# Kernel tuning notes

Hardware: AMD Instinct MI355X
Metric: run time of the kernel (lower is better)

## Reference

```python
import jax, jax.numpy as jnp
import numpy as np

N, E = 100_000, 1_600_000
NFEAT, NHID, HEADS = 128, 128, 2
FOUT = NHID // 2  # per-head out feats (DGL GATConv(nfeat, nhid//2, num_heads=2))
NEG_SLOPE = 0.2
LN_EPS = 1e-5


def setup_inputs() -> dict:
    key = jax.random.key(0)
    ks = jax.random.split(key, 10)
    h = jax.random.normal(ks[0], (N, NFEAT), dtype=jnp.float32)
    src = jax.random.randint(ks[1], (E,), 0, N, dtype=jnp.int32)
    dst = jax.random.randint(ks[2], (E,), 0, N, dtype=jnp.int32)
    # GATConv params
    W = jax.random.normal(ks[3], (NFEAT, HEADS * FOUT), dtype=jnp.float32) / np.sqrt(NFEAT)
    attn_l = jax.random.normal(ks[4], (HEADS, FOUT), dtype=jnp.float32) * 0.1
    attn_r = jax.random.normal(ks[5], (HEADS, FOUT), dtype=jnp.float32) * 0.1
    bias = jnp.zeros((HEADS * FOUT,), dtype=jnp.float32)
    # LayerNorm params
    gamma = jnp.ones((NHID,), dtype=jnp.float32)
    beta = jnp.zeros((NHID,), dtype=jnp.float32)
    return {"h": h, "src": src, "dst": dst, "W": W, "attn_l": attn_l,
            "attn_r": attn_r, "bias": bias, "gamma": gamma, "beta": beta}


def reference(h, src, dst, W, attn_l, attn_r, bias, gamma, beta):
    # --- GATConv ---
    feat = (h @ W).reshape(N, HEADS, FOUT)                 # [N,H,F]
    el = jnp.einsum('nhf,hf->nh', feat, attn_l)            # [N,H]
    er = jnp.einsum('nhf,hf->nh', feat, attn_r)            # [N,H]
    e = jax.nn.leaky_relu(el[src] + er[dst], NEG_SLOPE)    # [E,H]
    # edge softmax over incoming edges of each dst node
    emax = jax.ops.segment_max(e, dst, num_segments=N)     # [N,H] (-inf for empty ok)
    expe = jnp.exp(e - emax[dst])                          # [E,H]
    denom = jax.ops.segment_sum(expe, dst, num_segments=N) # [N,H]
    alpha = expe / denom[dst]                              # [E,H]
    msg = feat[src] * alpha[:, :, None]                    # [E,H,F]
    out = jax.ops.segment_sum(msg, dst, num_segments=N)    # [N,H,F]
    x = out.reshape(N, HEADS * FOUT) + bias                # [N,NHID]
    # --- LayerNorm ---
    mu = jnp.mean(x, axis=-1, keepdims=True)
    var = jnp.mean(jnp.square(x - mu), axis=-1, keepdims=True)
    return gamma * (x - mu) * jax.lax.rsqrt(var + LN_EPS) + beta
```

## Files before the change

kernel.cpp:

```cpp
#include <hip/hip_runtime.h>
#include <hip/hip_bf16.h>

#define NFEAT 128
#define NHID  128
#define HEADS 2
#define FOUT  64
#define NEG_SLOPE 0.2f
#define LN_EPS 1e-5f
#define MAXE 256
#define NPART 4
#define PACK_BLOCKS 64
#define STRIDE 64

typedef __attribute__((ext_vector_type(8))) short  short8;
typedef __attribute__((ext_vector_type(4))) float  floatx4;
typedef unsigned short ushort_t;

__device__ __forceinline__ unsigned short f32_to_bf16_bits(float x) {
    unsigned int u = __float_as_uint(x);
    unsigned int r = (u + 0x7FFF + ((u >> 16) & 1)) >> 16;
    return (unsigned short)r;
}

__global__ __launch_bounds__(256) void histscatter_pack_kernel(
    const float* __restrict__ W, ushort_t* __restrict__ pBhi,
    ushort_t* __restrict__ pBlo, const int* __restrict__ src,
    const int* __restrict__ dst, int* __restrict__ deg,
    int* __restrict__ csr_src, int E, int N)
{
    if (blockIdx.x < PACK_BLOCKS) {
        int i = blockIdx.x * 256 + threadIdx.x;
        int k = i >> 7, n = i & 127;
        float x = W[i];
        unsigned short hb = f32_to_bf16_bits(x);
        float hf = __uint_as_float(((unsigned int)hb) << 16);
        unsigned short lb = f32_to_bf16_bits(x - hf);
        int t = n >> 4, s = k >> 5, q = (k >> 3) & 3, j = k & 7;
        int lanei = (q << 4) | (n & 15);
        int idx = ((t * 4 + s) * 64 + lanei) * 8 + j;
        pBhi[idx] = hb; pBlo[idx] = lb;
        return;
    }
    int bid   = blockIdx.x - PACK_BLOCKS;
    int p     = bid & (NPART - 1);
    int chunk = bid >> 2;
    int i = chunk * 256 + threadIdx.x;
    if (i >= E) return;
    int d = dst[i];
    int lo = (int)(((long long)p       * N) / NPART);
    int hi = (int)(((long long)(p + 1) * N) / NPART);
    if (d >= lo && d < hi) {
        int pos = atomicAdd(&deg[d], 1);
        if (pos < STRIDE)
            csr_src[(size_t)d * STRIDE + pos] = src[i];
    }
}

__global__ __launch_bounds__(256) void gemm_mfma_kernel(
    const float* __restrict__ h,
    const ushort_t* __restrict__ pBhi, const ushort_t* __restrict__ pBlo,
    const float* __restrict__ attn_l, const float* __restrict__ attn_r,
    ushort_t* __restrict__ featb, float* __restrict__ el,
    float* __restrict__ er, int N)
{
    const int lane = threadIdx.x & 63;
    const int wv   = threadIdx.x >> 6;
    const int r0   = blockIdx.x * 64 + wv * 16;
    const int m    = lane & 15;
    const int q    = lane >> 4;
    int row  = r0 + m;
    int rowc = min(row, N - 1);
    const float* hrow = h + (size_t)rowc * NFEAT + q * 8;

    floatx4 acc[8];
#pragma unroll
    for (int t = 0; t < 8; t++) acc[t] = (floatx4){0.f, 0.f, 0.f, 0.f};

#pragma unroll
    for (int s = 0; s < 4; ++s) {
        float4 a0 = *(const float4*)(hrow + s * 32);
        float4 a1 = *(const float4*)(hrow + s * 32 + 4);
        float af[8] = {a0.x, a0.y, a0.z, a0.w, a1.x, a1.y, a1.z, a1.w};
        short8 ahi, alo;
#pragma unroll
        for (int jj = 0; jj < 8; jj++) {
            unsigned short hb = f32_to_bf16_bits(af[jj]);
            float hf = __uint_as_float(((unsigned int)hb) << 16);
            unsigned short lb = f32_to_bf16_bits(af[jj] - hf);
            ahi[jj] = (short)hb; alo[jj] = (short)lb;
        }
#pragma unroll
        for (int t = 0; t < 8; t++) {
            short8 bhi = *(const short8*)(pBhi + ((t * 4 + s) * 64 + lane) * 8);
            short8 blo = *(const short8*)(pBlo + ((t * 4 + s) * 64 + lane) * 8);
            acc[t] = __builtin_amdgcn_mfma_f32_16x16x32_bf16(ahi, bhi, acc[t], 0, 0, 0);
            acc[t] = __builtin_amdgcn_mfma_f32_16x16x32_bf16(ahi, blo, acc[t], 0, 0, 0);
            acc[t] = __builtin_amdgcn_mfma_f32_16x16x32_bf16(alo, bhi, acc[t], 0, 0, 0);
        }
    }
    if (r0 >= N) return;

    float alc[8], arc[8];
#pragma unroll
    for (int t = 0; t < 8; t++) {
        alc[t] = attn_l[t * 16 + m];
        arc[t] = attn_r[t * 16 + m];
    }

#pragma unroll
    for (int r = 0; r < 4; r++) {
        int rr = r0 + q * 4 + r;
        bool ok = (rr < N);
        if (ok) {
#pragma unroll
            for (int t = 0; t < 8; t++)
                featb[(size_t)rr * NHID + t * 16 + m] = f32_to_bf16_bits(acc[t][r]);
        }
        float pl0 = 0.f, pl1 = 0.f, pr0 = 0.f, pr1 = 0.f;
#pragma unroll
        for (int t = 0; t < 4; t++) {
            pl0 += acc[t][r] * alc[t];
            pr0 += acc[t][r] * arc[t];
            pl1 += acc[t + 4][r] * alc[t + 4];
            pr1 += acc[t + 4][r] * arc[t + 4];
        }
#pragma unroll
        for (int off = 1; off < 16; off <<= 1) {
            pl0 += __shfl_xor(pl0, off, 64);
            pl1 += __shfl_xor(pl1, off, 64);
            pr0 += __shfl_xor(pr0, off, 64);
            pr1 += __shfl_xor(pr1, off, 64);
        }
        if (m == 0 && ok) {
            el[rr * HEADS + 0] = pl0;
            el[rr * HEADS + 1] = pl1;
            er[rr * HEADS + 0] = pr0;
            er[rr * HEADS + 1] = pr1;
        }
    }
}

__global__ __launch_bounds__(256) void aggregate_kernel(
    const int* __restrict__ deg_arr, const int* __restrict__ csr_src,
    const ushort_t* __restrict__ featb, const float* __restrict__ el,
    const float* __restrict__ er, const float* __restrict__ bias,
    const float* __restrict__ gamma, const float* __restrict__ beta,
    float* __restrict__ out, int N)
{
    __shared__ int    s_src[4][STRIDE];
    __shared__ float2 s_e[4][STRIDE];

    const int wv   = threadIdx.x >> 6;
    const int lane = threadIdx.x & 63;
    const int node = blockIdx.x * 4 + wv;
    if (node >= N) return;

    const int deg = min(deg_arr[node], STRIDE);
    const int rs  = node * STRIDE;
    const float2 erv = *(const float2*)(er + (size_t)node * HEADS);

    float d0 = 0.f, d1 = 0.f;
    if (lane < deg) {
        int s = csr_src[rs + lane];
        float2 elv = *(const float2*)(el + (size_t)s * HEADS);
        float e0 = elv.x + erv.x; e0 = e0 > 0.f ? e0 : NEG_SLOPE * e0;
        float e1 = elv.y + erv.y; e1 = e1 > 0.f ? e1 : NEG_SLOPE * e1;
        float x0 = __expf(e0), x1 = __expf(e1);
        s_src[wv][lane] = s;
        s_e[wv][lane] = make_float2(x0, x1);
        d0 = x0; d1 = x1;
    }
#pragma unroll
    for (int off = 32; off; off >>= 1) {
        d0 += __shfl_xor(d0, off, 64);
        d1 += __shfl_xor(d1, off, 64);
    }

    const int j0   = lane * 2;
    const int hsel = lane >> 5;
    const float* s_ef = (const float*)&s_e[wv][0];
    float acc0 = 0.f, acc1 = 0.f;
    {
        int i = 0;
        for (; i + 8 <= deg; i += 8) {
            int s0 = s_src[wv][i + 0], s1 = s_src[wv][i + 1];
            int s2 = s_src[wv][i + 2], s3 = s_src[wv][i + 3];
            int s4 = s_src[wv][i + 4], s5 = s_src[wv][i + 5];
            int s6 = s_src[wv][i + 6], s7 = s_src[wv][i + 7];
            unsigned int u0 = *(const unsigned int*)(featb + (size_t)s0 * NHID + j0);
            unsigned int u1 = *(const unsigned int*)(featb + (size_t)s1 * NHID + j0);
            unsigned int u2 = *(const unsigned int*)(featb + (size_t)s2 * NHID + j0);
            unsigned int u3 = *(const unsigned int*)(featb + (size_t)s3 * NHID + j0);
            unsigned int u4 = *(const unsigned int*)(featb + (size_t)s4 * NHID + j0);
            unsigned int u5 = *(const unsigned int*)(featb + (size_t)s5 * NHID + j0);
            unsigned int u6 = *(const unsigned int*)(featb + (size_t)s6 * NHID + j0);
            unsigned int u7 = *(const unsigned int*)(featb + (size_t)s7 * NHID + j0);
            float a0 = s_ef[2 * (i + 0) + hsel];
            float a1 = s_ef[2 * (i + 1) + hsel];
            float a2 = s_ef[2 * (i + 2) + hsel];
            float a3 = s_ef[2 * (i + 3) + hsel];
            float a4 = s_ef[2 * (i + 4) + hsel];
            float a5 = s_ef[2 * (i + 5) + hsel];
            float a6 = s_ef[2 * (i + 6) + hsel];
            float a7 = s_ef[2 * (i + 7) + hsel];
            acc0 += __uint_as_float(u0 << 16) * a0;
            acc1 += __uint_as_float(u0 & 0xFFFF0000u) * a0;
            acc0 += __uint_as_float(u1 << 16) * a1;
            acc1 += __uint_as_float(u1 & 0xFFFF0000u) * a1;
            acc0 += __uint_as_float(u2 << 16) * a2;
            acc1 += __uint_as_float(u2 & 0xFFFF0000u) * a2;
            acc0 += __uint_as_float(u3 << 16) * a3;
            acc1 += __uint_as_float(u3 & 0xFFFF0000u) * a3;
            acc0 += __uint_as_float(u4 << 16) * a4;
            acc1 += __uint_as_float(u4 & 0xFFFF0000u) * a4;
            acc0 += __uint_as_float(u5 << 16) * a5;
            acc1 += __uint_as_float(u5 & 0xFFFF0000u) * a5;
            acc0 += __uint_as_float(u6 << 16) * a6;
            acc1 += __uint_as_float(u6 & 0xFFFF0000u) * a6;
            acc0 += __uint_as_float(u7 << 16) * a7;
            acc1 += __uint_as_float(u7 & 0xFFFF0000u) * a7;
        }
        for (; i + 2 <= deg; i += 2) {
            int s0 = s_src[wv][i + 0], s1 = s_src[wv][i + 1];
            unsigned int u0 = *(const unsigned int*)(featb + (size_t)s0 * NHID + j0);
            unsigned int u1 = *(const unsigned int*)(featb + (size_t)s1 * NHID + j0);
            float a0 = s_ef[2 * (i + 0) + hsel];
            float a1 = s_ef[2 * (i + 1) + hsel];
            acc0 += __uint_as_float(u0 << 16) * a0;
            acc1 += __uint_as_float(u0 & 0xFFFF0000u) * a0;
            acc0 += __uint_as_float(u1 << 16) * a1;
            acc1 += __uint_as_float(u1 & 0xFFFF0000u) * a1;
        }
        for (; i < deg; ++i) {
            int s = s_src[wv][i];
            float a = s_ef[2 * i + hsel];
            unsigned int u = *(const unsigned int*)(featb + (size_t)s * NHID + j0);
            acc0 += __uint_as_float(u << 16) * a;
            acc1 += __uint_as_float(u & 0xFFFF0000u) * a;
        }
    }
    float inv = (deg > 0) ? 1.f / ((lane < 32) ? d0 : d1) : 0.f;

    float2 bv = *(const float2*)(bias + j0);
    float x0 = acc0 * inv + bv.x;
    float x1 = acc1 * inv + bv.y;
    float s1 = x0 + x1, s2 = x0 * x0 + x1 * x1;
#pragma unroll
    for (int off = 32; off; off >>= 1) {
        s1 += __shfl_xor(s1, off, 64);
        s2 += __shfl_xor(s2, off, 64);
    }
    float mu  = s1 * (1.f / NHID);
    float var = s2 * (1.f / NHID) - mu * mu;
    float r   = rsqrtf(var + LN_EPS);
    float2 gv = *(const float2*)(gamma + j0);
    float2 tv = *(const float2*)(beta + j0);
    float2 yo = make_float2(gv.x * (x0 - mu) * r + tv.x,
                            gv.y * (x1 - mu) * r + tv.y);
    *(float2*)(out + (size_t)node * NHID + j0) = yo;
}

extern "C" void kernel_launch(void* const* d_in, const int* in_sizes, int n_in,
                              void* d_out, int out_size, void* d_ws, size_t ws_size,
                              hipStream_t stream)
{
    const float* h      = (const float*)d_in[0];
    const int*   src    = (const int*)  d_in[1];
    const int*   dst    = (const int*)  d_in[2];
    const float* W      = (const float*)d_in[3];
    const float* attn_l = (const float*)d_in[4];
    const float* attn_r = (const float*)d_in[5];
    const float* bias   = (const float*)d_in[6];
    const float* gamma  = (const float*)d_in[7];
    const float* beta   = (const float*)d_in[8];
    float* out = (float*)d_out;

    const int N = in_sizes[0] / NFEAT;
    const int E = in_sizes[1];
    const int NCHUNK = (E + 255) / 256;

    ushort_t* pBhi  = (ushort_t*)d_ws;
    ushort_t* pBlo  = pBhi + NFEAT * NHID;
    ushort_t* featb = pBlo + NFEAT * NHID;
    float* el       = (float*)(featb + (size_t)N * NHID);
    float* er       = el + (size_t)N * HEADS;
    int*   deg      = (int*)(er + (size_t)N * HEADS);
    int*   csr_src  = deg + N;

    hipMemsetAsync(deg, 0, (size_t)N * 4, stream);
    histscatter_pack_kernel<<<PACK_BLOCKS + NCHUNK * NPART, 256, 0, stream>>>(
        W, pBhi, pBlo, src, dst, deg, csr_src, E, N);

    gemm_mfma_kernel<<<(N + 63) / 64, 256, 0, stream>>>(h, pBhi, pBlo, attn_l,
                                                        attn_r, featb, el, er, N);
    aggregate_kernel<<<(N + 3) / 4, 256, 0, stream>>>(deg, csr_src, featb,
                                                      el, er, bias, gamma, beta,
                                                      out, N);
}
```

Measured before the change: 287.9 us.

## Split per-node degree counters into four groups to reduce atomic contention

After: 337.3 us. +17.1%, slower.

```diff
diff --git a/kernel.cpp b/kernel.cpp
--- a/kernel.cpp
+++ b/kernel.cpp
@@ -7,10 +7,11 @@
 #define FOUT  64
 #define NEG_SLOPE 0.2f
 #define LN_EPS 1e-5f
-#define MAXE 256
-#define NPART 4
+#define NGRP 4
+#define SUB  24
+#define ROW  (NGRP*SUB)
+#define MAXDEG 64
 #define PACK_BLOCKS 64
-#define STRIDE 64
 
 typedef __attribute__((ext_vector_type(8))) short  short8;
 typedef __attribute__((ext_vector_type(4))) float  floatx4;
@@ -25,7 +26,7 @@
 __global__ __launch_bounds__(256) void histscatter_pack_kernel(
     const float* __restrict__ W, ushort_t* __restrict__ pBhi,
     ushort_t* __restrict__ pBlo, const int* __restrict__ src,
-    const int* __restrict__ dst, int* __restrict__ deg,
+    const int* __restrict__ dst, int* __restrict__ deg_g,
     int* __restrict__ csr_src, int E, int N)
 {
     if (blockIdx.x < PACK_BLOCKS) {
@@ -41,19 +42,14 @@
         pBhi[idx] = hb; pBlo[idx] = lb;
         return;
     }
-    int bid   = blockIdx.x - PACK_BLOCKS;
-    int p     = bid & (NPART - 1);
-    int chunk = bid >> 2;
+    int chunk = blockIdx.x - PACK_BLOCKS;
     int i = chunk * 256 + threadIdx.x;
     if (i >= E) return;
+    int g = chunk & (NGRP - 1);
     int d = dst[i];
-    int lo = (int)(((long long)p       * N) / NPART);
-    int hi = (int)(((long long)(p + 1) * N) / NPART);
-    if (d >= lo && d < hi) {
-        int pos = atomicAdd(&deg[d], 1);
-        if (pos < STRIDE)
-            csr_src[(size_t)d * STRIDE + pos] = src[i];
-    }
+    int pos = atomicAdd(&deg_g[(size_t)g * N + d], 1);
+    if (pos < SUB)
+        csr_src[(size_t)d * ROW + g * SUB + pos] = src[i];
 }
 
 __global__ __launch_bounds__(256) void gemm_mfma_kernel(
@@ -141,27 +137,37 @@
 }
 
 __global__ __launch_bounds__(256) void aggregate_kernel(
-    const int* __restrict__ deg_arr, const int* __restrict__ csr_src,
+    const int* __restrict__ deg_g, const int* __restrict__ csr_src,
     const ushort_t* __restrict__ featb, const float* __restrict__ el,
     const float* __restrict__ er, const float* __restrict__ bias,
     const float* __restrict__ gamma, const float* __restrict__ beta,
     float* __restrict__ out, int N)
 {
-    __shared__ int    s_src[4][STRIDE];
-    __shared__ float2 s_e[4][STRIDE];
+    __shared__ int    s_src[4][MAXDEG];
+    __shared__ float2 s_e[4][MAXDEG];
 
     const int wv   = threadIdx.x >> 6;
     const int lane = threadIdx.x & 63;
     const int node = blockIdx.x * 4 + wv;
     if (node >= N) return;
 
-    const int deg = min(deg_arr[node], STRIDE);
-    const int rs  = node * STRIDE;
+    const int c0 = min(deg_g[(size_t)0 * N + node], SUB);
+    const int c1 = min(deg_g[(size_t)1 * N + node], SUB);
+    const int c2 = min(deg_g[(size_t)2 * N + node], SUB);
+    const int c3 = min(deg_g[(size_t)3 * N + node], SUB);
+    const int p1 = c0, p2 = c0 + c1, p3 = c0 + c1 + c2;
+    const int deg = min(p3 + c3, MAXDEG);
+    const size_t rs = (size_t)node * ROW;
     const float2 erv = *(const float2*)(er + (size_t)node * HEADS);
 
     float d0 = 0.f, d1 = 0.f;
     if (lane < deg) {
-        int s = csr_src[rs + lane];
+        int g = (lane >= p1) + (lane >= p2) + (lane >= p3);
+        int base = 0;
+        base = (g == 1) ? p1 : base;
+        base = (g == 2) ? p2 : base;
+        base = (g == 3) ? p3 : base;
+        int s = csr_src[rs + g * SUB + (lane - base)];
         float2 elv = *(const float2*)(el + (size_t)s * HEADS);
         float e0 = elv.x + erv.x; e0 = e0 > 0.f ? e0 : NEG_SLOPE * e0;
         float e1 = elv.y + erv.y; e1 = e1 > 0.f ? e1 : NEG_SLOPE * e1;
@@ -284,16 +290,16 @@
     ushort_t* featb = pBlo + NFEAT * NHID;
     float* el       = (float*)(featb + (size_t)N * NHID);
     float* er       = el + (size_t)N * HEADS;
-    int*   deg      = (int*)(er + (size_t)N * HEADS);
-    int*   csr_src  = deg + N;
-
-    hipMemsetAsync(deg, 0, (size_t)N * 4, stream);
-    histscatter_pack_kernel<<<PACK_BLOCKS + NCHUNK * NPART, 256, 0, stream>>>(
-        W, pBhi, pBlo, src, dst, deg, csr_src, E, N);
+    int*   deg_g    = (int*)(er + (size_t)N * HEADS);
+    int*   csr_src  = deg_g + (size_t)NGRP * N;
+
+    hipMemsetAsync(deg_g, 0, (size_t)NGRP * N * 4, stream);
+    histscatter_pack_kernel<<<PACK_BLOCKS + NCHUNK, 256, 0, stream>>>(
+        W, pBhi, pBlo, src, dst, deg_g, csr_src, E, N);
 
     gemm_mfma_kernel<<<(N + 63) / 64, 256, 0, stream>>>(h, pBhi, pBlo, attn_l,
                                                         attn_r, featb, el, er, N);
-    aggregate_kernel<<<(N + 3) / 4, 256, 0, stream>>>(deg, csr_src, featb,
+    aggregate_kernel<<<(N + 3) / 4, 256, 0, stream>>>(deg_g, csr_src, featb,
                                                       el, er, bias, gamma, beta,
                                                       out, N);
 }
```

## Replace global-atomic CSR build with two-pass bucketed binning via LDS atomics

Applied to the files above, without the earlier changes.

Result: faster. 245.9 us (-14.6%).

```diff
diff --git a/kernel.cpp b/kernel.cpp
--- a/kernel.cpp
+++ b/kernel.cpp
@@ -7,10 +7,12 @@
 #define FOUT  64
 #define NEG_SLOPE 0.2f
 #define LN_EPS 1e-5f
-#define MAXE 256
-#define NPART 4
 #define PACK_BLOCKS 64
 #define STRIDE 64
+#define EBLK 4096
+#define BSHIFT 9
+#define BSPAN 512
+#define BCAP 9216
 
 typedef __attribute__((ext_vector_type(8))) short  short8;
 typedef __attribute__((ext_vector_type(4))) float  floatx4;
@@ -22,14 +24,14 @@
     return (unsigned short)r;
 }
 
-__global__ __launch_bounds__(256) void histscatter_pack_kernel(
+__global__ __launch_bounds__(256) void bin_pack_kernel(
     const float* __restrict__ W, ushort_t* __restrict__ pBhi,
     ushort_t* __restrict__ pBlo, const int* __restrict__ src,
-    const int* __restrict__ dst, int* __restrict__ deg,
-    int* __restrict__ csr_src, int E, int N)
-{
-    if (blockIdx.x < PACK_BLOCKS) {
-        int i = blockIdx.x * 256 + threadIdx.x;
+    const int* __restrict__ dst, int* __restrict__ cursor,
+    int2* __restrict__ pairbuf, int E, int NCH1)
+{
+    if ((int)blockIdx.x >= NCH1) {
+        int i = ((int)blockIdx.x - NCH1) * 256 + threadIdx.x;
         int k = i >> 7, n = i & 127;
         float x = W[i];
         unsigned short hb = f32_to_bf16_bits(x);
@@ -41,19 +43,69 @@
         pBhi[idx] = hb; pBlo[idx] = lb;
         return;
     }
-    int bid   = blockIdx.x - PACK_BLOCKS;
-    int p     = bid & (NPART - 1);
-    int chunk = bid >> 2;
-    int i = chunk * 256 + threadIdx.x;
-    if (i >= E) return;
-    int d = dst[i];
-    int lo = (int)(((long long)p       * N) / NPART);
-    int hi = (int)(((long long)(p + 1) * N) / NPART);
-    if (d >= lo && d < hi) {
-        int pos = atomicAdd(&deg[d], 1);
-        if (pos < STRIDE)
-            csr_src[(size_t)d * STRIDE + pos] = src[i];
-    }
+
+    __shared__ int lcnt[256];
+    __shared__ int lbase[256];
+    const int t = threadIdx.x;
+    lcnt[t] = 0;
+    __syncthreads();
+
+    const int base = (int)blockIdx.x * EBLK + t * 16;
+    int sv[16], dv[16], rk[16];
+#pragma unroll
+    for (int g = 0; g < 4; g++) {
+        int o = base + g * 4;
+        if (o + 3 < E) {
+            int4 d4 = *(const int4*)(dst + o);
+            int4 s4 = *(const int4*)(src + o);
+            dv[g * 4 + 0] = d4.x; dv[g * 4 + 1] = d4.y;
+            dv[g * 4 + 2] = d4.z; dv[g * 4 + 3] = d4.w;
+            sv[g * 4 + 0] = s4.x; sv[g * 4 + 1] = s4.y;
+            sv[g * 4 + 2] = s4.z; sv[g * 4 + 3] = s4.w;
+        } else {
+#pragma unroll
+            for (int k = 0; k < 4; k++) {
+                int i = o + k;
+                dv[g * 4 + k] = (i < E) ? dst[i] : -1;
+                sv[g * 4 + k] = (i < E) ? src[i] : 0;
+            }
+        }
+    }
+#pragma unroll
+    for (int k = 0; k < 16; k++)
+        rk[k] = (dv[k] >= 0) ? atomicAdd(&lcnt[dv[k] >> BSHIFT], 1) : 0;
+    __syncthreads();
+    lbase[t] = (lcnt[t] > 0) ? atomicAdd(&cursor[t * 16], lcnt[t]) : 0;
+    __syncthreads();
+#pragma unroll
+    for (int k = 0; k < 16; k++) {
+        if (dv[k] >= 0) {
+            int b = dv[k] >> BSHIFT;
+            int pos = lbase[b] + rk[k];
+            if (pos < BCAP)
+                pairbuf[(size_t)b * BCAP + pos] = make_int2(sv[k], dv[k]);
+        }
+    }
+}
+
+__global__ __launch_bounds__(1024) void place_kernel(
+    const int2* __restrict__ pairbuf, const int* __restrict__ cursor,
+    int* __restrict__ deg, int* __restrict__ csr_src, int N)
+{
+    __shared__ int lcnt[BSPAN];
+    const int b = blockIdx.x, t = threadIdx.x;
+    if (t < BSPAN) lcnt[t] = 0;
+    __syncthreads();
+    const int nlo = b << BSHIFT;
+    const int cnt = min(cursor[b * 16], BCAP);
+    for (int i = t; i < cnt; i += 1024) {
+        int2 p = pairbuf[(size_t)b * BCAP + i];
+        int r = atomicAdd(&lcnt[p.y - nlo], 1);
+        if (r < STRIDE)
+            csr_src[(size_t)p.y * STRIDE + r] = p.x;
+    }
+    __syncthreads();
+    if (t < BSPAN && nlo + t < N) deg[nlo + t] = lcnt[t];
 }
 
 __global__ __launch_bounds__(256) void gemm_mfma_kernel(
@@ -277,7 +329,8 @@
 
     const int N = in_sizes[0] / NFEAT;
     const int E = in_sizes[1];
-    const int NCHUNK = (E + 255) / 256;
+    const int NCH1 = (E + EBLK - 1) / EBLK;
+    const int NBUK = (N + BSPAN - 1) >> BSHIFT;
 
     ushort_t* pBhi  = (ushort_t*)d_ws;
     ushort_t* pBlo  = pBhi + NFEAT * NHID;
@@ -286,10 +339,13 @@
     float* er       = el + (size_t)N * HEADS;
     int*   deg      = (int*)(er + (size_t)N * HEADS);
     int*   csr_src  = deg + N;
-
-    hipMemsetAsync(deg, 0, (size_t)N * 4, stream);
-    histscatter_pack_kernel<<<PACK_BLOCKS + NCHUNK * NPART, 256, 0, stream>>>(
-        W, pBhi, pBlo, src, dst, deg, csr_src, E, N);
+    int*   cursor   = csr_src + (size_t)N * STRIDE;
+    int2*  pairbuf  = (int2*)(cursor + (size_t)NBUK * 16);
+
+    hipMemsetAsync(cursor, 0, (size_t)NBUK * 16 * 4, stream);
+    bin_pack_kernel<<<NCH1 + PACK_BLOCKS, 256, 0, stream>>>(
+        W, pBhi, pBlo, src, dst, cursor, pairbuf, E, NCH1);
+    place_kernel<<<NBUK, 1024, 0, stream>>>(pairbuf, cursor, deg, csr_src, N);
 
     gemm_mfma_kernel<<<(N + 63) / 64, 256, 0, stream>>>(h, pBhi, pBlo, attn_l,
                                                         attn_r, featb, el, er, N);
```
